# Kernel tuning notes

Measured on AMD Instinct MI355X. Metric: run time of the kernel, lower is better.

The kernel has to match this reference:

```python
import jax, jax.numpy as jnp
import numpy as np

BN_EPS = 1e-5

def _bn(h, g, b):
    # training-mode BatchNorm1d over the node/graph axis (biased variance)
    m = jnp.mean(h, axis=0)
    v = jnp.mean((h - m) ** 2, axis=0)
    return (h - m) * jax.lax.rsqrt(v + BN_EPS) * g + b

def setup_inputs() -> dict:
    N, E, H, L, G = 100000, 1600000, 128, 3, 512
    key = jax.random.key(0)
    ks = jax.random.split(key, 24)
    x = jax.random.normal(ks[0], (N, H), dtype=jnp.float32)
    edge_index = jax.random.randint(ks[1], (2, E), 0, N, dtype=jnp.int64)
    batch = jnp.sort(jax.random.randint(ks[2], (N,), 0, G, dtype=jnp.int64))
    s = 0.05
    inp = {
        "x": x, "edge_index": edge_index, "batch": batch, "num_graphs": G,
        # stacked per-layer GINConv MLP params: Linear(H,2H)->BN(2H)->ReLU->Linear(2H,H)
        "conv_w1": jax.random.normal(ks[3], (L, H, 2 * H), jnp.float32) * s,
        "conv_b1": jnp.zeros((L, 2 * H), jnp.float32),
        "conv_bn_g": jnp.ones((L, 2 * H), jnp.float32),
        "conv_bn_b": jnp.zeros((L, 2 * H), jnp.float32),
        "conv_w2": jax.random.normal(ks[4], (L, 2 * H, H), jnp.float32) * s,
        "conv_b2": jnp.zeros((L, H), jnp.float32),
        # outer per-layer BatchNorm1d(H)
        "bn_g": jnp.ones((L, H), jnp.float32),
        "bn_b": jnp.zeros((L, H), jnp.float32),
        # virtual node embedding (nn.Embedding(1, H))
        "vn_emb": jax.random.normal(ks[5], (H,), jnp.float32) * s,
        # virtual MLP: Linear(H,2H)->BN->ReLU->Linear(2H,H)->BN->ReLU
        "vmlp_w1": jax.random.normal(ks[6], (H, 2 * H), jnp.float32) * s,
        "vmlp_b1": jnp.zeros((2 * H,), jnp.float32),
        "vmlp_bn1_g": jnp.ones((2 * H,), jnp.float32),
        "vmlp_bn1_b": jnp.zeros((2 * H,), jnp.float32),
        "vmlp_w2": jax.random.normal(ks[7], (2 * H, H), jnp.float32) * s,
        "vmlp_b2": jnp.zeros((H,), jnp.float32),
        "vmlp_bn2_g": jnp.ones((H,), jnp.float32),
        "vmlp_bn2_b": jnp.zeros((H,), jnp.float32),
    }
    return inp

def reference(x, edge_index, batch, num_graphs, conv_w1, conv_b1, conv_bn_g, conv_bn_b,
              conv_w2, conv_b2, bn_g, bn_b, vn_emb, vmlp_w1, vmlp_b1, vmlp_bn1_g,
              vmlp_bn1_b, vmlp_w2, vmlp_b2, vmlp_bn2_g, vmlp_bn2_b):
    N = x.shape[0]
    L = conv_w1.shape[0]
    src, dst = edge_index[0], edge_index[1]

    vf = jnp.broadcast_to(vn_emb, (num_graphs, vn_emb.shape[0]))  # [G, H]
    feats = x
    for i in range(L):
        h = feats + vf[batch] if i > 0 else feats
        # GINConv (eps=0): MLP(x + sum_{j in N(i)} x_j); scatter-add over edges
        agg = jax.ops.segment_sum(h[src], dst, num_segments=N)
        z = h + agg
        z = jax.nn.relu(_bn(z @ conv_w1[i] + conv_b1[i], conv_bn_g[i], conv_bn_b[i]))
        z = z @ conv_w2[i] + conv_b2[i]
        z = _bn(z, bn_g[i], bn_b[i])
        if i < L - 1:
            z = jax.nn.relu(z)
        feats = z  # dropout is identity (eval / rate=0)
        if 0 < i < L - 1:
            pooled = jax.ops.segment_sum(feats, batch, num_segments=num_graphs)
            v = pooled + vf
            v = jax.nn.relu(_bn(v @ vmlp_w1 + vmlp_b1, vmlp_bn1_g, vmlp_bn1_b))
            v = jax.nn.relu(_bn(v @ vmlp_w2 + vmlp_b2, vmlp_bn2_g, vmlp_bn2_b))
            vf = v

    # global mean pool readout
    graph_sum = jax.ops.segment_sum(feats, batch, num_segments=num_graphs)
    counts = jax.ops.segment_sum(jnp.ones((N,), feats.dtype), batch, num_segments=num_graphs)
    out_readout = graph_sum / jnp.clip(counts, 1.0)[:, None]
    return feats, out_readout, vf
```

## Files before the change

kernel.cpp:

```cpp
#include <hip/hip_runtime.h>


#define HDIM 128
#define H2DIM 256
#define GNUM 512
#define BN_EPS 1e-5f

typedef short bf16x8 __attribute__((ext_vector_type(8)));
typedef float f32x4 __attribute__((ext_vector_type(4)));

__device__ __forceinline__ unsigned short f2bf(float f) {
  unsigned int u = __float_as_uint(f);
  u = (u + 0x7FFFu + ((u >> 16) & 1u)) >> 16;
  return (unsigned short)u;
}
__device__ __forceinline__ float bf2f(unsigned short s) {
  return __uint_as_float(((unsigned int)s) << 16);
}


__global__ __launch_bounds__(256) void k_init_vf(const float* __restrict__ emb,
                                                 float* __restrict__ vf) {
  int idx = blockIdx.x * 256 + threadIdx.x;
  if (idx < GNUM * HDIM) vf[idx] = emb[idx & (HDIM - 1)];
}

__global__ __launch_bounds__(256) void k_h_init(const float* __restrict__ feats,
                                                const float* __restrict__ vf,
                                                const int* __restrict__ batch,
                                                unsigned short* __restrict__ h,
                                                int N, int useVf) {
  int idx = blockIdx.x * 256 + threadIdx.x;
  int total = N * (HDIM / 4);
  if (idx >= total) return;
  int n = idx >> 5;
  int c4 = idx & 31;
  float4 v = ((const float4*)feats)[idx];
  if (useVf) {
    int g = batch[n];
    float4 w = ((const float4*)(vf + (size_t)g * HDIM))[c4];
    v.x += w.x; v.y += w.y; v.z += w.z; v.w += w.w;
  }
  ushort4 o;
  o.x = f2bf(v.x); o.y = f2bf(v.y); o.z = f2bf(v.z); o.w = f2bf(v.w);
  ((ushort4*)h)[idx] = o;
}

__global__ __launch_bounds__(256) void k_bnfuse(const float* __restrict__ Y,
                                                const float* __restrict__ scale,
                                                const float* __restrict__ shift,
                                                const float* __restrict__ vf,
                                                const int* __restrict__ batch,
                                                unsigned short* __restrict__ hout,
                                                int N) {
  int idx = blockIdx.x * 256 + threadIdx.x;
  int total = N * (HDIM / 4);
  if (idx >= total) return;
  int n = idx >> 5;
  int c4 = idx & 31;
  int c = c4 * 4;
  float4 v = ((const float4*)Y)[idx];
  int g = batch[n];
  float4 w = ((const float4*)(vf + (size_t)g * HDIM))[c4];
  v.x = fmaxf(fmaf(v.x, scale[c + 0], shift[c + 0]), 0.f) + w.x;
  v.y = fmaxf(fmaf(v.y, scale[c + 1], shift[c + 1]), 0.f) + w.y;
  v.z = fmaxf(fmaf(v.z, scale[c + 2], shift[c + 2]), 0.f) + w.z;
  v.w = fmaxf(fmaf(v.w, scale[c + 3], shift[c + 3]), 0.f) + w.w;
  ushort4 o;
  o.x = f2bf(v.x); o.y = f2bf(v.y); o.z = f2bf(v.z); o.w = f2bf(v.w);
  ((ushort4*)hout)[idx] = o;
}

__global__ __launch_bounds__(256) void k_convw_all(const float* __restrict__ w1,
                                                   const float* __restrict__ w2,
                                                   unsigned short* __restrict__ wt1,
                                                   unsigned short* __restrict__ wt2) {
  int idx = blockIdx.x * 256 + threadIdx.x;
  const int P = 3 * HDIM * H2DIM;
  if (idx < P) {
    int i = idx / (H2DIM * HDIM);
    int o = idx % (H2DIM * HDIM);
    int n = o / HDIM;
    int k = o % HDIM;
    wt1[idx] = f2bf(w1[(size_t)i * HDIM * H2DIM + (size_t)k * H2DIM + n]);
  } else if (idx < 2 * P) {
    int o2 = idx - P;
    int i = o2 / (HDIM * H2DIM);
    int o = o2 % (HDIM * H2DIM);
    int n = o / H2DIM;
    int k = o % H2DIM;
    wt2[o2] = f2bf(w2[(size_t)i * H2DIM * HDIM + (size_t)k * HDIM + n]);
  }
}


__global__ __launch_bounds__(256) void k_hist(const int* __restrict__ ei,
                                              int* __restrict__ deg, int E) {
  int e = blockIdx.x * 256 + threadIdx.x;
  if (e < E) atomicAdd(&deg[ei[E + e]], 1);
}

__global__ __launch_bounds__(256) void k_scan1(const int* __restrict__ deg,
                                               int* __restrict__ bsum, int N) {
  __shared__ int sh[256];
  int t = threadIdx.x;
  int base = blockIdx.x * 2048 + t * 8;
  int s = 0;
#pragma unroll
  for (int j = 0; j < 8; ++j) {
    int i = base + j;
    if (i < N) s += deg[i];
  }
  sh[t] = s;
  __syncthreads();
  for (int off = 128; off > 0; off >>= 1) {
    if (t < off) sh[t] += sh[t + off];
    __syncthreads();
  }
  if (t == 0) bsum[blockIdx.x] = sh[0];
}

__global__ __launch_bounds__(256) void k_scan2(int* __restrict__ bsum, int nb,
                                               int* __restrict__ row_ptr, int N) {
  __shared__ int sh[256];
  int t = threadIdx.x;
  int v = (t < nb) ? bsum[t] : 0;
  sh[t] = v;
  __syncthreads();
  for (int off = 1; off < 256; off <<= 1) {
    int add = (t >= off) ? sh[t - off] : 0;
    __syncthreads();
    sh[t] += add;
    __syncthreads();
  }
  if (t < nb) bsum[t] = sh[t] - v;
  if (t == 255) row_ptr[N] = sh[255];
}

__global__ __launch_bounds__(256) void k_scan3(const int* __restrict__ deg,
                                               const int* __restrict__ boff,
                                               int* __restrict__ row_ptr, int N) {
  __shared__ int sh[256];
  int t = threadIdx.x;
  int base = blockIdx.x * 2048 + t * 8;
  int d[8];
  int s = 0;
#pragma unroll
  for (int j = 0; j < 8; ++j) {
    int i = base + j;
    d[j] = (i < N) ? deg[i] : 0;
    s += d[j];
  }
  sh[t] = s;
  __syncthreads();
  for (int off = 1; off < 256; off <<= 1) {
    int add = (t >= off) ? sh[t - off] : 0;
    __syncthreads();
    sh[t] += add;
    __syncthreads();
  }
  int run = boff[blockIdx.x] + sh[t] - s;
#pragma unroll
  for (int j = 0; j < 8; ++j) {
    int i = base + j;
    if (i < N) {
      row_ptr[i] = run;
      run += d[j];
    }
  }
}

__global__ __launch_bounds__(256) void k_binA(const int* __restrict__ ei,
                                              const int* __restrict__ row_ptr,
                                              int* __restrict__ bktcur,
                                              int* __restrict__ staged,
                                              int E, int NB) {
  __shared__ int hist[512];
  __shared__ int lbase[512];
  int tid = threadIdx.x;
  hist[tid] = 0; hist[tid + 256] = 0;
  __syncthreads();
  int e0 = blockIdx.x * 4096;
#pragma unroll
  for (int j = 0; j < 16; ++j) {
    int e = e0 + j * 256 + tid;
    if (e < E) atomicAdd(&hist[ei[E + e] >> 8], 1);
  }
  __syncthreads();
  for (int t = tid; t < NB; t += 256) {
    int cgot = hist[t];
    if (cgot > 0) lbase[t] = row_ptr[t << 8] + atomicAdd(&bktcur[t], cgot);
    hist[t] = 0;
  }
  __syncthreads();
#pragma unroll
  for (int j = 0; j < 16; ++j) {
    int e = e0 + j * 256 + tid;
    if (e < E) {
      int d = ei[E + e];
      int b = d >> 8;
      int loc = atomicAdd(&hist[b], 1);
      staged[lbase[b] + loc] = (ei[e] << 8) | (d & 255);
    }
  }
}

__global__ __launch_bounds__(256) void k_binB(const int* __restrict__ row_ptr,
                                              const int* __restrict__ staged,
                                              int* __restrict__ csr, int N) {
  __shared__ int lcur[256];
  int b = blockIdx.x;
  int node0 = b << 8;
  int tid = threadIdx.x;
  int nend = min(node0 + 256, N);
  lcur[tid] = (node0 + tid < N) ? row_ptr[node0 + tid] : 0;
  __syncthreads();
  int s0 = row_ptr[node0];
  int s1 = row_ptr[nend];
  for (int j = s0 + tid; j < s1; j += 256) {
    int rec = staged[j];
    int pos = atomicAdd(&lcur[rec & 255], 1);
    csr[pos] = rec >> 8;
  }
}

__device__ __forceinline__ void acc8(float* a, uint4 v) {
  a[0] += bf2f((unsigned short)v.x); a[1] += bf2f((unsigned short)(v.x >> 16));
  a[2] += bf2f((unsigned short)v.y); a[3] += bf2f((unsigned short)(v.y >> 16));
  a[4] += bf2f((unsigned short)v.z); a[5] += bf2f((unsigned short)(v.z >> 16));
  a[6] += bf2f((unsigned short)v.w); a[7] += bf2f((unsigned short)(v.w >> 16));
}

__global__ __launch_bounds__(256) void k_aggregate(const unsigned short* __restrict__ h,
                                                   const int* __restrict__ row_ptr,
                                                   const int* __restrict__ csr,
                                                   unsigned short* __restrict__ z,
                                                   int N) {
  int n = blockIdx.x * 16 + (threadIdx.x >> 4);
  if (n >= N) return;
  int lane = threadIdx.x & 15;
  const uint4* __restrict__ hp = (const uint4*)h;
  float a[8];
  {
    uint4 u = hp[(size_t)n * 16 + lane];
    a[0] = bf2f((unsigned short)u.x); a[1] = bf2f((unsigned short)(u.x >> 16));
    a[2] = bf2f((unsigned short)u.y); a[3] = bf2f((unsigned short)(u.y >> 16));
    a[4] = bf2f((unsigned short)u.z); a[5] = bf2f((unsigned short)(u.z >> 16));
    a[6] = bf2f((unsigned short)u.w); a[7] = bf2f((unsigned short)(u.w >> 16));
  }
  int beg = row_ptr[n], end = row_ptr[n + 1];
  int j = beg;
  for (; j + 4 <= end; j += 4) {
    int s0 = csr[j], s1 = csr[j + 1], s2 = csr[j + 2], s3 = csr[j + 3];
    uint4 v0 = hp[(size_t)s0 * 16 + lane];
    uint4 v1 = hp[(size_t)s1 * 16 + lane];
    uint4 v2 = hp[(size_t)s2 * 16 + lane];
    uint4 v3 = hp[(size_t)s3 * 16 + lane];
    acc8(a, v0); acc8(a, v1); acc8(a, v2); acc8(a, v3);
  }
  for (; j < end; ++j) {
    uint4 v = hp[(size_t)csr[j] * 16 + lane];
    acc8(a, v);
  }
  uint4 o;
  o.x = (unsigned int)f2bf(a[0]) | ((unsigned int)f2bf(a[1]) << 16);
  o.y = (unsigned int)f2bf(a[2]) | ((unsigned int)f2bf(a[3]) << 16);
  o.z = (unsigned int)f2bf(a[4]) | ((unsigned int)f2bf(a[5]) << 16);
  o.w = (unsigned int)f2bf(a[6]) | ((unsigned int)f2bf(a[7]) << 16);
  ((uint4*)z)[(size_t)n * 16 + lane] = o;
}

#define LDA_S 76
__global__ __launch_bounds__(256) void k_gemm_mfma(
    const unsigned short* __restrict__ A, const unsigned short* __restrict__ Wt,
    const float* __restrict__ bias, const float* __restrict__ kscale,
    const float* __restrict__ kshift, void* __restrict__ Cout, int outBf16,
    float* __restrict__ pS, float* __restrict__ pQ, int mblocks,
    int M, int K, int Nc) {
  __shared__ unsigned short As[64 * LDA_S];
  __shared__ unsigned short Bs[128 * LDA_S];
  __shared__ float redS[128];
  __shared__ float redQ[128];
  __shared__ float ksc[256];
  __shared__ float ksh[256];

  int tid = threadIdx.x;
  int lane = tid & 63;
  int wid = tid >> 6;
  int wrow = (wid & 1) * 32;
  int wcol = (wid >> 1) * 64;
  int bm = blockIdx.x * 64;
  int bn = blockIdx.y * 128;
  int lrow = lane & 15;
  int lkg = lane >> 4;

  if (tid < 128) { redS[tid] = 0.f; redQ[tid] = 0.f; }
  if (kscale) {
    for (int k = tid; k < K; k += 256) { ksc[k] = kscale[k]; ksh[k] = kshift[k]; }
  }

  f32x4 acc[2][4];
#pragma unroll
  for (int r = 0; r < 2; ++r)
#pragma unroll
    for (int c = 0; c < 4; ++c) acc[r][c] = (f32x4){0.f, 0.f, 0.f, 0.f};

  for (int kt = 0; kt < K; kt += 64) {
    __syncthreads();
#pragma unroll
    for (int it = 0; it < 2; ++it) {
      int ga = it * 256 + tid;
      int row = ga >> 3;
      int g = ga & 7;
      int k0 = kt + g * 8;
      bf16x8 av = (bf16x8){0, 0, 0, 0, 0, 0, 0, 0};
      int grow = bm + row;
      if (grow < M) av = *(const bf16x8*)(A + (size_t)grow * K + k0);
      if (kscale) {
#pragma unroll
        for (int j = 0; j < 8; ++j) {
          float f = bf2f((unsigned short)av[j]);
          f = fmaxf(fmaf(f, ksc[k0 + j], ksh[k0 + j]), 0.f);
          av[j] = (short)f2bf(f);
        }
      }
      *(bf16x8*)(As + row * LDA_S + g * 8) = av;
    }
#pragma unroll
    for (int it = 0; it < 4; ++it) {
      int gb = it * 256 + tid;
      int row = gb >> 3;
      int g = gb & 7;
      bf16x8 bv = *(const bf16x8*)(Wt + (size_t)(bn + row) * K + kt + g * 8);
      *(bf16x8*)(Bs + row * LDA_S + g * 8) = bv;
    }
    __syncthreads();
#pragma unroll
    for (int ks = 0; ks < 2; ++ks) {
      int goff = ks * 4 + lkg;
      bf16x8 af[2], bfr[4];
#pragma unroll
      for (int rf = 0; rf < 2; ++rf)
        af[rf] = *(const bf16x8*)(As + (wrow + rf * 16 + lrow) * LDA_S + goff * 8);
#pragma unroll
      for (int cf = 0; cf < 4; ++cf)
        bfr[cf] = *(const bf16x8*)(Bs + (wcol + cf * 16 + lrow) * LDA_S + goff * 8);
#pragma unroll
      for (int rf = 0; rf < 2; ++rf)
#pragma unroll
        for (int cf = 0; cf < 4; ++cf)
          acc[rf][cf] = __builtin_amdgcn_mfma_f32_16x16x32_bf16(
              af[rf], bfr[cf], acc[rf][cf], 0, 0, 0);
    }
  }

#pragma unroll
  for (int cf = 0; cf < 4; ++cf) {
    int lcol = wcol + cf * 16 + lrow;
    float bb = bias[bn + lcol];
    float s = 0.f, q = 0.f;
#pragma unroll
    for (int rf = 0; rf < 2; ++rf) {
#pragma unroll
      for (int j = 0; j < 4; ++j) {
        float v = acc[rf][cf][j] + bb;
        acc[rf][cf][j] = v;
        int grow = bm + wrow + rf * 16 + lkg * 4 + j;
        if (grow < M) { s += v; q += v * v; }
      }
    }
    s += __shfl_xor(s, 16); s += __shfl_xor(s, 32);
    q += __shfl_xor(q, 16); q += __shfl_xor(q, 32);
    if (lane < 16) {
      atomicAdd(&redS[lcol], s);
      atomicAdd(&redQ[lcol], q);
    }
  }

#pragma unroll
  for (int cf = 0; cf < 4; ++cf) {
    int col = bn + wcol + cf * 16 + lrow;
#pragma unroll
    for (int rf = 0; rf < 2; ++rf) {
#pragma unroll
      for (int j = 0; j < 4; ++j) {
        int grow = bm + wrow + rf * 16 + lkg * 4 + j;
        if (grow < M) {
          float v = acc[rf][cf][j];
          if (outBf16)
            ((unsigned short*)Cout)[(size_t)grow * Nc + col] = f2bf(v);
          else
            ((float*)Cout)[(size_t)grow * Nc + col] = v;
        }
      }
    }
  }
  __syncthreads();
  if (tid < 128) {
    size_t off = (size_t)(bn + tid) * mblocks + blockIdx.x;
    pS[off] = redS[tid];
    pQ[off] = redQ[tid];
  }
}

__global__ __launch_bounds__(256) void k_bnfin2(const float* __restrict__ pS,
                                                const float* __restrict__ pQ,
                                                const float* __restrict__ g,
                                                const float* __restrict__ b,
                                                float* __restrict__ scale,
                                                float* __restrict__ shift,
                                                int mblocks, float invM) {
  __shared__ float shS[256], shQ[256];
  int c = blockIdx.x;
  int t = threadIdx.x;
  const float* rs = pS + (size_t)c * mblocks;
  const float* rq = pQ + (size_t)c * mblocks;
  float s = 0.f, q = 0.f;
  for (int j = t; j < mblocks; j += 256) { s += rs[j]; q += rq[j]; }
  shS[t] = s; shQ[t] = q;
  __syncthreads();
  for (int off = 128; off > 0; off >>= 1) {
    if (t < off) { shS[t] += shS[t + off]; shQ[t] += shQ[t + off]; }
    __syncthreads();
  }
  if (t == 0) {
    float mean = shS[0] * invM;
    float var = shQ[0] * invM - mean * mean;
    float inv = rsqrtf(var + BN_EPS);
    float sc = g[c] * inv;
    scale[c] = sc;
    shift[c] = fmaf(-mean, sc, b[c]);
  }
}

__global__ __launch_bounds__(256) void k_gemm(const float* __restrict__ A,
                                              const float* __restrict__ B,
                                              const float* __restrict__ bias,
                                              const float* __restrict__ kscale,
                                              const float* __restrict__ kshift,
                                              float* __restrict__ C,
                                              int M, int K, int Nc) {
  __shared__ float As[16][65];
  __shared__ float Bs[16][65];
  int tid = threadIdx.x;
  int bm = blockIdx.x * 64;
  int bn = blockIdx.y * 64;
  int trow = (tid >> 4) << 2;
  int tcol = (tid & 15) << 2;
  float acc[4][4] = {};

  int arow = tid >> 2;
  int ak = (tid & 3) << 2;
  int bt4 = tid << 2;
  int bk = bt4 >> 6;
  int bcol = bt4 & 63;

  for (int kt = 0; kt < K; kt += 16) {
    float4 av = make_float4(0.f, 0.f, 0.f, 0.f);
    int grow = bm + arow;
    if (grow < M) av = *(const float4*)(A + (size_t)grow * K + kt + ak);
    if (kscale) {
      int k0 = kt + ak;
      av.x = fmaxf(fmaf(av.x, kscale[k0 + 0], kshift[k0 + 0]), 0.f);
      av.y = fmaxf(fmaf(av.y, kscale[k0 + 1], kshift[k0 + 1]), 0.f);
      av.z = fmaxf(fmaf(av.z, kscale[k0 + 2], kshift[k0 + 2]), 0.f);
      av.w = fmaxf(fmaf(av.w, kscale[k0 + 3], kshift[k0 + 3]), 0.f);
    }
    float4 bv = *(const float4*)(B + (size_t)(kt + bk) * Nc + bn + bcol);
    __syncthreads();
    As[ak + 0][arow] = av.x;
    As[ak + 1][arow] = av.y;
    As[ak + 2][arow] = av.z;
    As[ak + 3][arow] = av.w;
    Bs[bk][bcol + 0] = bv.x;
    Bs[bk][bcol + 1] = bv.y;
    Bs[bk][bcol + 2] = bv.z;
    Bs[bk][bcol + 3] = bv.w;
    __syncthreads();
#pragma unroll
    for (int k = 0; k < 16; ++k) {
      float a0 = As[k][trow + 0], a1 = As[k][trow + 1];
      float a2 = As[k][trow + 2], a3 = As[k][trow + 3];
      float b0 = Bs[k][tcol + 0], b1 = Bs[k][tcol + 1];
      float b2 = Bs[k][tcol + 2], b3 = Bs[k][tcol + 3];
      acc[0][0] = fmaf(a0, b0, acc[0][0]); acc[0][1] = fmaf(a0, b1, acc[0][1]);
      acc[0][2] = fmaf(a0, b2, acc[0][2]); acc[0][3] = fmaf(a0, b3, acc[0][3]);
      acc[1][0] = fmaf(a1, b0, acc[1][0]); acc[1][1] = fmaf(a1, b1, acc[1][1]);
      acc[1][2] = fmaf(a1, b2, acc[1][2]); acc[1][3] = fmaf(a1, b3, acc[1][3]);
      acc[2][0] = fmaf(a2, b0, acc[2][0]); acc[2][1] = fmaf(a2, b1, acc[2][1]);
      acc[2][2] = fmaf(a2, b2, acc[2][2]); acc[2][3] = fmaf(a2, b3, acc[2][3]);
      acc[3][0] = fmaf(a3, b0, acc[3][0]); acc[3][1] = fmaf(a3, b1, acc[3][1]);
      acc[3][2] = fmaf(a3, b2, acc[3][2]); acc[3][3] = fmaf(a3, b3, acc[3][3]);
    }
  }
#pragma unroll
  for (int r = 0; r < 4; ++r) {
    int grow = bm + trow + r;
    if (grow < M) {
      float4 o;
      o.x = acc[r][0] + bias[bn + tcol + 0];
      o.y = acc[r][1] + bias[bn + tcol + 1];
      o.z = acc[r][2] + bias[bn + tcol + 2];
      o.w = acc[r][3] + bias[bn + tcol + 3];
      *(float4*)(C + (size_t)grow * Nc + bn + tcol) = o;
    }
  }
}


__global__ void k_colstats(const float* __restrict__ Y, int M, int C, int stripe,
                           float* __restrict__ sum, float* __restrict__ sumsq) {
  int c = threadIdx.x;
  int r0 = blockIdx.x * stripe;
  int r1 = min(r0 + stripe, M);
  float s = 0.f, ss = 0.f;
  for (int r = r0; r < r1; ++r) {
    float v = Y[(size_t)r * C + c];
    s += v; ss += v * v;
  }
  atomicAdd(&sum[c], s);
  atomicAdd(&sumsq[c], ss);
}

__global__ void k_bnfin(const float* __restrict__ sum, const float* __restrict__ sumsq,
                        const float* __restrict__ g, const float* __restrict__ b,
                        float* __restrict__ scale, float* __restrict__ shift,
                        int C, float invM) {
  int c = threadIdx.x;
  if (c >= C) return;
  float mean = sum[c] * invM;
  float var = sumsq[c] * invM - mean * mean;
  float inv = rsqrtf(var + BN_EPS);
  float sc = g[c] * inv;
  scale[c] = sc;
  shift[c] = fmaf(-mean, sc, b[c]);
}

__global__ __launch_bounds__(256) void k_bnapply(const float* __restrict__ Y,
                                                 const float* __restrict__ scale,
                                                 const float* __restrict__ shift,
                                                 float* __restrict__ out,
                                                 long long total4, int Cq, int relu) {
  long long idx = (long long)blockIdx.x * 256 + threadIdx.x;
  if (idx >= total4) return;
  int c = (int)(idx % Cq) * 4;
  float4 v = ((const float4*)Y)[idx];
  v.x = fmaf(v.x, scale[c + 0], shift[c + 0]);
  v.y = fmaf(v.y, scale[c + 1], shift[c + 1]);
  v.z = fmaf(v.z, scale[c + 2], shift[c + 2]);
  v.w = fmaf(v.w, scale[c + 3], shift[c + 3]);
  if (relu) {
    v.x = fmaxf(v.x, 0.f); v.y = fmaxf(v.y, 0.f);
    v.z = fmaxf(v.z, 0.f); v.w = fmaxf(v.w, 0.f);
  }
  ((float4*)out)[idx] = v;
}


__global__ __launch_bounds__(256) void k_pool2(const float* __restrict__ X,
                                               const int* __restrict__ batch,
                                               float* __restrict__ pooled,
                                               float* __restrict__ counts, int N) {
  int c = threadIdx.x & 127;
  int half = threadIdx.x >> 7;
  int base = blockIdx.x * 128 + half * 64;
  if (base >= N) return;
  int lim = min(64, N - base);
  int g = batch[base];
  float acc = 0.f, cnt = 0.f;
  for (int r = 0; r < lim; ++r) {
    int bg = batch[base + r];
    if (bg != g) {
      atomicAdd(&pooled[(size_t)g * HDIM + c], acc);
      if (c == 0 && counts) atomicAdd(&counts[g], cnt);
      acc = 0.f; cnt = 0.f; g = bg;
    }
    acc += X[(size_t)(base + r) * HDIM + c];
    cnt += 1.f;
  }
  atomicAdd(&pooled[(size_t)g * HDIM + c], acc);
  if (c == 0 && counts) atomicAdd(&counts[g], cnt);
}

__global__ __launch_bounds__(256) void k_add(const float* __restrict__ a,
                                             const float* __restrict__ b,
                                             float* __restrict__ o, int n) {
  int idx = blockIdx.x * 256 + threadIdx.x;
  if (idx < n) o[idx] = a[idx] + b[idx];
}

__global__ __launch_bounds__(256) void k_readout(const float* __restrict__ pooled,
                                                 const float* __restrict__ counts,
                                                 float* __restrict__ out, int n) {
  int idx = blockIdx.x * 256 + threadIdx.x;
  if (idx >= n) return;
  int g = idx >> 7;
  out[idx] = pooled[idx] / fmaxf(counts[g], 1.0f);
}


extern "C" void kernel_launch(void* const* d_in, const int* in_sizes, int n_in,
                              void* d_out, int out_size, void* d_ws, size_t ws_size,
                              hipStream_t stream) {
  const float* x       = (const float*)d_in[0];
  const int*   ei      = (const int*)d_in[1];
  const int*   batch   = (const int*)d_in[2];
  const float* conv_w1 = (const float*)d_in[4];
  const float* conv_b1 = (const float*)d_in[5];
  const float* conv_bng = (const float*)d_in[6];
  const float* conv_bnb = (const float*)d_in[7];
  const float* conv_w2 = (const float*)d_in[8];
  const float* conv_b2 = (const float*)d_in[9];
  const float* bn_g    = (const float*)d_in[10];
  const float* bn_b    = (const float*)d_in[11];
  const float* vn_emb  = (const float*)d_in[12];
  const float* vw1     = (const float*)d_in[13];
  const float* vb1     = (const float*)d_in[14];
  const float* vbn1g   = (const float*)d_in[15];
  const float* vbn1b   = (const float*)d_in[16];
  const float* vw2     = (const float*)d_in[17];
  const float* vb2     = (const float*)d_in[18];
  const float* vbn2g   = (const float*)d_in[19];
  const float* vbn2b   = (const float*)d_in[20];

  const int N = in_sizes[2];
  const int E = in_sizes[1] / 2;
  const int L = 3;

  const size_t NH  = (size_t)N * HDIM;
  const size_t NH2 = (size_t)N * H2DIM;

  float*          y2   = (float*)d_ws;
  unsigned short* h_b  = (unsigned short*)d_ws;
  unsigned short* z_b  = h_b + NH;
  unsigned short* y1_b = z_b + NH;
  unsigned short* wt1b = y1_b + NH2;
  unsigned short* wt2b = wt1b + (size_t)3 * H2DIM * HDIM;
  float* sum1   = (float*)(wt2b + (size_t)3 * HDIM * H2DIM);
  float* ss1    = sum1 + H2DIM;
  float* sum2   = ss1 + H2DIM;
  float* ss2    = sum2 + HDIM;
  float* scale1 = ss2 + HDIM;
  float* shift1 = scale1 + H2DIM;
  float* scale2 = shift1 + H2DIM;
  float* shift2 = scale2 + HDIM;
  float* vf     = shift2 + HDIM;
  float* pooled = vf + (size_t)GNUM * HDIM;
  float* vin    = pooled + (size_t)GNUM * HDIM;
  float* v1     = vin + (size_t)GNUM * HDIM;
  float* counts = v1 + (size_t)GNUM * H2DIM;
  int*   cursor = (int*)(counts + GNUM);
  int*   bktcur = cursor + N;
  int*   row_ptr = bktcur + 512;
  int*   csr    = row_ptr + N + 1;
  int*   staged = csr + E;
  int*   bsum   = staged + E;
  unsigned short* hb2 = (unsigned short*)(bsum + 256);

  const int mblocks = (N + 63) / 64;
  float* pS = (float*)staged;
  float* pQ = pS + (size_t)256 * mblocks;

  float* out_feats = (float*)d_out;
  float* out_read  = out_feats + NH;
  float* out_vf    = out_read + (size_t)GNUM * HDIM;

  dim3 blk(256);
  const int gridNH4 = (int)((NH / 4 + 255) / 256);
  const int gridE = (E + 255) / 256;
  const int nb = (N + 2047) / 2048;
  const int NB = (N + 255) >> 8;

  hipMemsetAsync(cursor, 0, (size_t)(N + 512) * sizeof(int), stream);
  k_hist<<<gridE, blk, 0, stream>>>(ei, cursor, E);
  k_scan1<<<nb, blk, 0, stream>>>(cursor, bsum, N);
  k_scan2<<<1, blk, 0, stream>>>(bsum, nb, row_ptr, N);
  k_scan3<<<nb, blk, 0, stream>>>(cursor, bsum, row_ptr, N);
  k_binA<<<(E + 4095) / 4096, blk, 0, stream>>>(ei, row_ptr, bktcur, staged, E, NB);
  k_binB<<<NB, blk, 0, stream>>>(row_ptr, staged, csr, N);

  k_convw_all<<<(2 * 3 * HDIM * H2DIM + 255) / 256, blk, 0, stream>>>(
      conv_w1, conv_w2, wt1b, wt2b);

  k_init_vf<<<(GNUM * HDIM + 255) / 256, blk, 0, stream>>>(vn_emb, vf);

  for (int i = 0; i < L; ++i) {
    if (i == 0)
      k_h_init<<<gridNH4, blk, 0, stream>>>(x, vf, batch, h_b, N, 0);
    else if (i == 2)
      k_h_init<<<gridNH4, blk, 0, stream>>>(out_feats, vf, batch, h_b, N, 1);
    const unsigned short* hcur = (i == 1) ? hb2 : h_b;

    k_aggregate<<<(N + 15) / 16, blk, 0, stream>>>(hcur, row_ptr, csr, z_b, N);

    k_gemm_mfma<<<dim3(mblocks, H2DIM / 128), blk, 0, stream>>>(
        z_b, wt1b + (size_t)i * H2DIM * HDIM, conv_b1 + (size_t)i * H2DIM,
        nullptr, nullptr, y1_b, 1, pS, pQ, mblocks, N, HDIM, H2DIM);
    k_bnfin2<<<H2DIM, blk, 0, stream>>>(pS, pQ, conv_bng + (size_t)i * H2DIM,
                                        conv_bnb + (size_t)i * H2DIM,
                                        scale1, shift1, mblocks, 1.0f / N);

    k_gemm_mfma<<<dim3(mblocks, HDIM / 128), blk, 0, stream>>>(
        y1_b, wt2b + (size_t)i * HDIM * H2DIM, conv_b2 + (size_t)i * HDIM,
        scale1, shift1, y2, 0, pS, pQ, mblocks, N, H2DIM, HDIM);
    k_bnfin2<<<HDIM, blk, 0, stream>>>(pS, pQ, bn_g + (size_t)i * HDIM,
                                       bn_b + (size_t)i * HDIM,
                                       scale2, shift2, mblocks, 1.0f / N);

    if (i == 0) {
      k_bnfuse<<<gridNH4, blk, 0, stream>>>(y2, scale2, shift2, vf, batch, hb2, N);
    } else {
      k_bnapply<<<gridNH4, blk, 0, stream>>>(y2, scale2, shift2, out_feats,
                                             (long long)(NH / 4), HDIM / 4,
                                             (i < L - 1) ? 1 : 0);
    }

    if (i == 1) {
      hipMemsetAsync(pooled, 0, (size_t)GNUM * HDIM * sizeof(float), stream);
      k_pool2<<<(N + 127) / 128, blk, 0, stream>>>(out_feats, batch, pooled,
                                                   nullptr, N);
      k_add<<<(GNUM * HDIM + 255) / 256, blk, 0, stream>>>(pooled, vf, vin,
                                                           GNUM * HDIM);

      hipMemsetAsync(sum1, 0, (size_t)(2 * H2DIM + 2 * HDIM) * sizeof(float), stream);
      k_gemm<<<dim3(GNUM / 64, H2DIM / 64), blk, 0, stream>>>(
          vin, vw1, vb1, nullptr, nullptr, v1, GNUM, HDIM, H2DIM);
      k_colstats<<<(GNUM + 127) / 128, H2DIM, 0, stream>>>(v1, GNUM, H2DIM, 128,
                                                           sum1, ss1);
      k_bnfin<<<1, H2DIM, 0, stream>>>(sum1, ss1, vbn1g, vbn1b, scale1, shift1,
                                       H2DIM, 1.0f / GNUM);

      k_gemm<<<dim3(GNUM / 64, HDIM / 64), blk, 0, stream>>>(
          v1, vw2, vb2, scale1, shift1, vin, GNUM, H2DIM, HDIM);
      k_colstats<<<(GNUM + 127) / 128, HDIM, 0, stream>>>(vin, GNUM, HDIM, 128,
                                                          sum2, ss2);
      k_bnfin<<<1, HDIM, 0, stream>>>(sum2, ss2, vbn2g, vbn2b, scale2, shift2,
                                      HDIM, 1.0f / GNUM);
      k_bnapply<<<(GNUM * HDIM / 4 + 255) / 256, blk, 0, stream>>>(
          vin, scale2, shift2, vf, (long long)(GNUM * HDIM / 4), HDIM / 4, 1);
    }
  }

  hipMemsetAsync(pooled, 0, (size_t)GNUM * HDIM * sizeof(float), stream);
  hipMemsetAsync(counts, 0, (size_t)GNUM * sizeof(float), stream);
  k_pool2<<<(N + 127) / 128, blk, 0, stream>>>(out_feats, batch, pooled, counts, N);
  k_readout<<<(GNUM * HDIM + 255) / 256, blk, 0, stream>>>(pooled, counts, out_read,
                                                           GNUM * HDIM);
  hipMemcpyAsync(out_vf, vf, (size_t)GNUM * HDIM * sizeof(float),
                 hipMemcpyDeviceToDevice, stream);
}
```

Measured before the change: 793.7 us.

## Split neighbor aggregation into column slabs across grid y for cache locality

The CSR gather-sum aggregation is restructured so each block covers 128 nodes but only a 32-byte column slab (2 lanes × 16 bytes) selected by blockIdx.y over 8 slabs. Before, 16 lanes read each full 256-byte row. Slicing the feature matrix by column shrinks the working set per slab so gathered neighbor rows are more likely to hit in L2/MALL. CSR indices are read and the output written with nontemporal hints to avoid polluting the cache. In exchange, each edge index is now read 8 times instead of once and each gather is a narrower, less coalesced access, and the unroll drops from 4 to 2.

```diff
diff --git a/kernel.cpp b/kernel.cpp
--- a/kernel.cpp
+++ b/kernel.cpp
@@ -8,6 +8,7 @@
 
 typedef short bf16x8 __attribute__((ext_vector_type(8)));
 typedef float f32x4 __attribute__((ext_vector_type(4)));
+typedef unsigned int u32x4 __attribute__((ext_vector_type(4)));
 
 __device__ __forceinline__ unsigned short f2bf(float f) {
   unsigned int u = __float_as_uint(f);
@@ -224,25 +225,25 @@
   }
 }
 
-__device__ __forceinline__ void acc8(float* a, uint4 v) {
+__device__ __forceinline__ void acc8v(float* a, u32x4 v) {
   a[0] += bf2f((unsigned short)v.x); a[1] += bf2f((unsigned short)(v.x >> 16));
   a[2] += bf2f((unsigned short)v.y); a[3] += bf2f((unsigned short)(v.y >> 16));
   a[4] += bf2f((unsigned short)v.z); a[5] += bf2f((unsigned short)(v.z >> 16));
   a[6] += bf2f((unsigned short)v.w); a[7] += bf2f((unsigned short)(v.w >> 16));
 }
 
-__global__ __launch_bounds__(256) void k_aggregate(const unsigned short* __restrict__ h,
-                                                   const int* __restrict__ row_ptr,
-                                                   const int* __restrict__ csr,
-                                                   unsigned short* __restrict__ z,
-                                                   int N) {
-  int n = blockIdx.x * 16 + (threadIdx.x >> 4);
+__global__ __launch_bounds__(256) void k_aggp(const unsigned short* __restrict__ h,
+                                              const int* __restrict__ row_ptr,
+                                              const int* __restrict__ csr,
+                                              unsigned short* __restrict__ z,
+                                              int N) {
+  int n = blockIdx.x * 128 + (threadIdx.x >> 1);
   if (n >= N) return;
-  int lane = threadIdx.x & 15;
-  const uint4* __restrict__ hp = (const uint4*)h;
+  size_t coloff = (size_t)blockIdx.y * 2 + (threadIdx.x & 1);
+  const u32x4* __restrict__ hp = (const u32x4*)h;
   float a[8];
   {
-    uint4 u = hp[(size_t)n * 16 + lane];
+    u32x4 u = hp[(size_t)n * 16 + coloff];
     a[0] = bf2f((unsigned short)u.x); a[1] = bf2f((unsigned short)(u.x >> 16));
     a[2] = bf2f((unsigned short)u.y); a[3] = bf2f((unsigned short)(u.y >> 16));
     a[4] = bf2f((unsigned short)u.z); a[5] = bf2f((unsigned short)(u.z >> 16));
@@ -250,24 +251,23 @@
   }
   int beg = row_ptr[n], end = row_ptr[n + 1];
   int j = beg;
-  for (; j + 4 <= end; j += 4) {
-    int s0 = csr[j], s1 = csr[j + 1], s2 = csr[j + 2], s3 = csr[j + 3];
-    uint4 v0 = hp[(size_t)s0 * 16 + lane];
-    uint4 v1 = hp[(size_t)s1 * 16 + lane];
-    uint4 v2 = hp[(size_t)s2 * 16 + lane];
-    uint4 v3 = hp[(size_t)s3 * 16 + lane];
-    acc8(a, v0); acc8(a, v1); acc8(a, v2); acc8(a, v3);
-  }
-  for (; j < end; ++j) {
-    uint4 v = hp[(size_t)csr[j] * 16 + lane];
-    acc8(a, v);
-  }
-  uint4 o;
+  for (; j + 2 <= end; j += 2) {
+    int s0 = __builtin_nontemporal_load(&csr[j]);
+    int s1 = __builtin_nontemporal_load(&csr[j + 1]);
+    u32x4 v0 = hp[(size_t)s0 * 16 + coloff];
+    u32x4 v1 = hp[(size_t)s1 * 16 + coloff];
+    acc8v(a, v0); acc8v(a, v1);
+  }
+  if (j < end) {
+    int s = __builtin_nontemporal_load(&csr[j]);
+    acc8v(a, hp[(size_t)s * 16 + coloff]);
+  }
+  u32x4 o;
   o.x = (unsigned int)f2bf(a[0]) | ((unsigned int)f2bf(a[1]) << 16);
   o.y = (unsigned int)f2bf(a[2]) | ((unsigned int)f2bf(a[3]) << 16);
   o.z = (unsigned int)f2bf(a[4]) | ((unsigned int)f2bf(a[5]) << 16);
   o.w = (unsigned int)f2bf(a[6]) | ((unsigned int)f2bf(a[7]) << 16);
-  ((uint4*)z)[(size_t)n * 16 + lane] = o;
+  __builtin_nontemporal_store(o, (u32x4*)z + (size_t)n * 16 + coloff);
 }
 
 #define LDA_S 76
@@ -670,6 +670,7 @@
   const int gridE = (E + 255) / 256;
   const int nb = (N + 2047) / 2048;
   const int NB = (N + 255) >> 8;
+  const dim3 gridAgg((N + 127) / 128, 8);
 
   hipMemsetAsync(cursor, 0, (size_t)(N + 512) * sizeof(int), stream);
   k_hist<<<gridE, blk, 0, stream>>>(ei, cursor, E);
@@ -691,7 +692,7 @@
       k_h_init<<<gridNH4, blk, 0, stream>>>(out_feats, vf, batch, h_b, N, 1);
     const unsigned short* hcur = (i == 1) ? hb2 : h_b;
 
-    k_aggregate<<<(N + 15) / 16, blk, 0, stream>>>(hcur, row_ptr, csr, z_b, N);
+    k_aggp<<<gridAgg, blk, 0, stream>>>(hcur, row_ptr, csr, z_b, N);
 
     k_gemm_mfma<<<dim3(mblocks, H2DIM / 128), blk, 0, stream>>>(
         z_b, wt1b + (size_t)i * H2DIM * HDIM, conv_b1 + (size_t)i * H2DIM,
```

Measured after the change: 1.406 ms. 77.1% more time.
